# Performance work log

Measured on AMD Instinct MI355X. Metric: run time of the kernel, lower is better.

Reference implementation:

```python
import jax, jax.numpy as jnp
import numpy as np

HEAD_SIZE = 128
NUM_EMBED = 1024
BLOCK_SIZE = 2048


def setup_inputs() -> dict:
    key = jax.random.key(0)
    kx, kk, kq, kv = jax.random.split(key, 4)
    x = jax.random.normal(kx, (4, BLOCK_SIZE, NUM_EMBED), dtype=jnp.float32)
    s = 1.0 / np.sqrt(NUM_EMBED)
    Wk = jax.random.normal(kk, (NUM_EMBED, HEAD_SIZE), dtype=jnp.float32) * s
    Wq = jax.random.normal(kq, (NUM_EMBED, HEAD_SIZE), dtype=jnp.float32) * s
    Wv = jax.random.normal(kv, (NUM_EMBED, HEAD_SIZE), dtype=jnp.float32) * s
    return {"x": x, "Wk": Wk, "Wq": Wq, "Wv": Wv}


def reference(x, Wk, Wq, Wv):
    # x: [B, T, C]; W*: [C, H]
    B, T, C = x.shape
    k = x @ Wk          # [B, T, H]
    q = x @ Wq          # [B, T, H]
    v = x @ Wv          # [B, T, H]
    scale = k.shape[-1] ** -0.5
    wei = jnp.einsum('bth,bsh->bts', q, k) * scale  # [B, T, T]
    causal = jnp.tril(jnp.ones((T, T), dtype=bool))
    wei = jnp.where(causal, wei, -jnp.inf)
    wei = jax.nn.softmax(wei, axis=-1)
    out = jnp.einsum('bts,bsh->bth', wei, v)        # [B, T, H]
    return out
```

## Files before the change

### kernel.cpp

```cpp
#include <hip/hip_runtime.h>
#include <hip/hip_bf16.h>
#include <math.h>

#define B_ 4
#define T_ 2048
#define C_ 1024
#define H_ 128
#define SCALE 0.088388347648318447f

typedef unsigned short u16;
typedef __bf16 bf16x8 __attribute__((ext_vector_type(8)));
typedef __bf16 bf16x4 __attribute__((ext_vector_type(4)));
typedef float  f32x4  __attribute__((ext_vector_type(4)));
typedef u16    u16x8  __attribute__((ext_vector_type(8)));
typedef u16    u16x4  __attribute__((ext_vector_type(4)));

#define PO_OFF  0u
#define ML_OFF  18874368u
#define WBT_OFF 19169280u
#define QB_OFF  19955712u
#define KB_OFF  22052864u
#define VT_OFF  24150016u

__device__ __forceinline__ u16 f2bf(float f) {
    __hip_bfloat16 h = __float2bfloat16(f);
    return __builtin_bit_cast(u16, h);
}

__device__ __forceinline__ void load_lds16(const void* g, void* l) {
    __builtin_amdgcn_global_load_lds(
        (const __attribute__((address_space(1))) unsigned int*)g,
        (__attribute__((address_space(3))) unsigned int*)l, 16, 0, 0);
}

__global__ __launch_bounds__(256) void convert_w(const float* __restrict__ Wq,
                                                 const float* __restrict__ Wk,
                                                 const float* __restrict__ Wv,
                                                 u16* __restrict__ wbT) {
    const int id = blockIdx.x * 256 + threadIdx.x;
    const int s = id >> 17;
    const int r = id & 131071;
    const int k = r >> 7, n = r & 127;
    const float* W = (s == 0) ? Wq : (s == 1) ? Wk : Wv;
    float v = W[k * 128 + n];
    if (s == 0) v *= SCALE;
    wbT[(s << 17) + (n << 10) + k] = f2bf(v);
}

__global__ __launch_bounds__(256) void gemm_qkv(
    const float* __restrict__ x, const u16* __restrict__ wbT,
    u16* __restrict__ qb, u16* __restrict__ kb, u16* __restrict__ vT)
{
    __shared__ u16 xs[2][4096];
    __shared__ u16 ws[2][8192];

    const int tid = threadIdx.x;
    const int w = tid >> 6, lane = tid & 63, lg = lane >> 4, lr = lane & 15;
    const int wm = w >> 1, wn = w & 1;
    const int s = blockIdx.y;
    const int m0 = blockIdx.x * 64;
    const u16* wsrc = wbT + (s << 17);

    const int xrow = tid >> 2;
    const int xseg = tid & 3;
    const float* xbase = x + (size_t)(m0 + xrow) * C_ + xseg * 16;
    const unsigned xsw = ((unsigned)xrow & 7u) << 4;

    unsigned wro[4], wco[4];
#pragma unroll
    for (int i = 0; i < 4; ++i) {
        const unsigned o = (unsigned)(w * 4 + i) * 1024u + (unsigned)lane * 16u;
        const unsigned o2 = o ^ (((o >> 7) & 7u) << 4);
        wro[i] = o2 >> 7; wco[i] = (o2 & 127u) >> 1;
    }

    f32x4 acc[2][4] = {};

    {
        const float4 f0 = ((const float4*)xbase)[0], f1 = ((const float4*)xbase)[1];
        const float4 f2 = ((const float4*)xbase)[2], f3 = ((const float4*)xbase)[3];
#pragma unroll
        for (int i = 0; i < 4; ++i)
            load_lds16(wsrc + (size_t)wro[i] * C_ + wco[i], &ws[0][(w * 4 + i) * 512]);
        u16x8 lo, hi;
        lo[0] = f2bf(f0.x); lo[1] = f2bf(f0.y); lo[2] = f2bf(f0.z); lo[3] = f2bf(f0.w);
        lo[4] = f2bf(f1.x); lo[5] = f2bf(f1.y); lo[6] = f2bf(f1.z); lo[7] = f2bf(f1.w);
        hi[0] = f2bf(f2.x); hi[1] = f2bf(f2.y); hi[2] = f2bf(f2.z); hi[3] = f2bf(f2.w);
        hi[4] = f2bf(f3.x); hi[5] = f2bf(f3.y); hi[6] = f2bf(f3.z); hi[7] = f2bf(f3.w);
        char* rb = (char*)xs[0] + xrow * 128;
        *(u16x8*)(rb + (((unsigned)xseg * 32 + 0) ^ xsw)) = lo;
        *(u16x8*)(rb + (((unsigned)xseg * 32 + 16) ^ xsw)) = hi;
    }
    __syncthreads();

    int buf = 0;
    for (int k0 = 0; k0 < C_; k0 += 64) {
        const bool pf = (k0 + 64 < C_);
        float4 g0, g1, g2, g3;
        if (pf) {
            const float* xn = xbase + k0 + 64;
            g0 = ((const float4*)xn)[0]; g1 = ((const float4*)xn)[1];
            g2 = ((const float4*)xn)[2]; g3 = ((const float4*)xn)[3];
#pragma unroll
            for (int i = 0; i < 4; ++i)
                load_lds16(wsrc + (size_t)wro[i] * C_ + (k0 + 64) + wco[i],
                           &ws[buf ^ 1][(w * 4 + i) * 512]);
        }

#pragma unroll
        for (int kc = 0; kc < 2; ++kc) {
            bf16x8 af[2], bfr[4];
#pragma unroll
            for (int mi = 0; mi < 2; ++mi) {
                const int row = wm * 32 + mi * 16 + lr;
                const unsigned byte = (unsigned)(kc * 64 + lg * 16) ^ (((unsigned)row & 7u) << 4);
                af[mi] = *(const bf16x8*)((const char*)xs[buf] + row * 128 + byte);
            }
#pragma unroll
            for (int ni = 0; ni < 4; ++ni) {
                const int n = wn * 64 + ni * 16 + lr;
                const unsigned byte = (unsigned)(kc * 64 + lg * 16) ^ (((unsigned)n & 7u) << 4);
                bfr[ni] = *(const bf16x8*)((const char*)ws[buf] + n * 128 + byte);
            }
#pragma unroll
            for (int mi = 0; mi < 2; ++mi)
#pragma unroll
                for (int ni = 0; ni < 4; ++ni)
                    acc[mi][ni] = __builtin_amdgcn_mfma_f32_16x16x32_bf16(
                        af[mi], bfr[ni], acc[mi][ni], 0, 0, 0);
        }

        if (pf) {
            u16x8 lo, hi;
            lo[0] = f2bf(g0.x); lo[1] = f2bf(g0.y); lo[2] = f2bf(g0.z); lo[3] = f2bf(g0.w);
            lo[4] = f2bf(g1.x); lo[5] = f2bf(g1.y); lo[6] = f2bf(g1.z); lo[7] = f2bf(g1.w);
            hi[0] = f2bf(g2.x); hi[1] = f2bf(g2.y); hi[2] = f2bf(g2.z); hi[3] = f2bf(g2.w);
            hi[4] = f2bf(g3.x); hi[5] = f2bf(g3.y); hi[6] = f2bf(g3.z); hi[7] = f2bf(g3.w);
            char* rb = (char*)xs[buf ^ 1] + xrow * 128;
            *(u16x8*)(rb + (((unsigned)xseg * 32 + 0) ^ xsw)) = lo;
            *(u16x8*)(rb + (((unsigned)xseg * 32 + 16) ^ xsw)) = hi;
        }
        __syncthreads();
        buf ^= 1;
    }

    if (s < 2) {
        u16* dst = (s == 0) ? qb : kb;
#pragma unroll
        for (int mi = 0; mi < 2; ++mi)
#pragma unroll
            for (int ni = 0; ni < 4; ++ni) {
                const int trow = m0 + wm * 32 + mi * 16 + lg * 4;
                const int col = wn * 64 + ni * 16 + lr;
#pragma unroll
                for (int r = 0; r < 4; ++r)
                    dst[(size_t)(trow + r) * H_ + col] = f2bf(acc[mi][ni][r]);
            }
    } else {
#pragma unroll
        for (int mi = 0; mi < 2; ++mi)
#pragma unroll
            for (int ni = 0; ni < 4; ++ni) {
                const int trow = m0 + wm * 32 + mi * 16 + lg * 4;
                const int bb = trow >> 11, t = trow & 2047;
                const int d = wn * 64 + ni * 16 + lr;
                u16x4 pk;
                pk[0] = f2bf(acc[mi][ni][0]); pk[1] = f2bf(acc[mi][ni][1]);
                pk[2] = f2bf(acc[mi][ni][2]); pk[3] = f2bf(acc[mi][ni][3]);
                *(u16x4*)&vT[((size_t)bb * 128 + d) * 2048 + t] = pk;
            }
    }
}

__global__ __launch_bounds__(256) void attn_split(
    const u16* __restrict__ qb, const u16* __restrict__ kb,
    const u16* __restrict__ vT, float* __restrict__ po, float* __restrict__ ml)
{
    __shared__ u16 ks[2][4096];
    __shared__ u16 vs[2][128 * 36];

    const int jt = blockIdx.x, sp = blockIdx.y, b = blockIdx.z;
    const int kt0 = sp * 8;
    const int ktend_all = 2 * jt + 2;
    if (kt0 >= ktend_all) return;
    const int kt_end = min(kt0 + 8, ktend_all);

    const int tid = threadIdx.x;
    const int w = tid >> 6, lane = tid & 63, lg = lane >> 4, lr = lane & 15;
    const int qrow_base = jt * 64 + w * 16;

    const u16* kbB = kb + ((size_t)(b << 11)) * H_;
    const u16* vbB = vT + (size_t)b * 128 * 2048;

    unsigned krow[2], kcolb[2];
#pragma unroll
    for (int i = 0; i < 2; ++i) {
        const unsigned o_ = (unsigned)(w * 2 + i) * 1024u + (unsigned)lane * 16u;
        const unsigned o2 = o_ ^ (((o_ >> 8) & 7u) << 4);
        krow[i] = o2 >> 8; kcolb[i] = o2 & 255u;
    }
    int vd[2], vc[2];
#pragma unroll
    for (int i = 0; i < 2; ++i) {
        const int idx = i * 256 + tid;
        vd[i] = idx >> 2; vc[i] = idx & 3;
    }

    const u16* qp = qb + ((size_t)(b << 11) + qrow_base + lr) * H_;
    bf16x8 qf[4];
#pragma unroll
    for (int kc = 0; kc < 4; ++kc)
        qf[kc] = *(const bf16x8*)&qp[kc * 32 + lg * 8];

    u16x8 vr[2];
    {
        const u16* kbase = kbB + (size_t)kt0 * 32 * H_;
#pragma unroll
        for (int i = 0; i < 2; ++i)
            load_lds16((const char*)kbase + krow[i] * 256 + kcolb[i], &ks[0][(w * 2 + i) * 512]);
        const u16* vbase = vbB + (size_t)kt0 * 32;
#pragma unroll
        for (int i = 0; i < 2; ++i)
            vr[i] = *(const u16x8*)&vbase[(size_t)vd[i] * 2048 + vc[i] * 8];
#pragma unroll
        for (int i = 0; i < 2; ++i) {
            char* rb = (char*)vs[0] + vd[i] * 72 + (vc[i] & 2) * 4;
            *(u16x4*)(rb + ((2 * vc[i]) & 3) * 16)     = __builtin_shufflevector(vr[i], vr[i], 0, 1, 2, 3);
            *(u16x4*)(rb + ((2 * vc[i] + 1) & 3) * 16) = __builtin_shufflevector(vr[i], vr[i], 4, 5, 6, 7);
        }
    }
    __syncthreads();

    f32x4 o[8] = {};
    float m_run = -INFINITY, l_run = 0.f;
    int cur = 0;

    for (int kt = kt0; kt < kt_end; ++kt) {
        const bool pf = (kt + 1 < kt_end);
        if (pf) {
            const u16* kbase = kbB + (size_t)(kt + 1) * 32 * H_;
#pragma unroll
            for (int i = 0; i < 2; ++i)
                load_lds16((const char*)kbase + krow[i] * 256 + kcolb[i],
                           &ks[cur ^ 1][(w * 2 + i) * 512]);
            const u16* vbase = vbB + (size_t)(kt + 1) * 32;
#pragma unroll
            for (int i = 0; i < 2; ++i)
                vr[i] = *(const u16x8*)&vbase[(size_t)vd[i] * 2048 + vc[i] * 8];
        }

        f32x4 s0 = {0.f, 0.f, 0.f, 0.f}, s1 = {0.f, 0.f, 0.f, 0.f};
        const unsigned swz = ((unsigned)lr & 7u) << 4;
#pragma unroll
        for (int kc = 0; kc < 4; ++kc) {
            const unsigned byte = ((unsigned)(kc * 64 + lg * 16)) ^ swz;
            const bf16x8 kf0 = *(const bf16x8*)((const char*)ks[cur] + lr * 256 + byte);
            const bf16x8 kf1 = *(const bf16x8*)((const char*)ks[cur] + lr * 256 + 4096 + byte);
            s0 = __builtin_amdgcn_mfma_f32_16x16x32_bf16(kf0, qf[kc], s0, 0, 0, 0);
            s1 = __builtin_amdgcn_mfma_f32_16x16x32_bf16(kf1, qf[kc], s1, 0, 0, 0);
        }

        if (kt * 32 + 31 > qrow_base) {
            const int qg = qrow_base + lr;
            const int kvb = kt * 32 + lg * 4;
#pragma unroll
            for (int r = 0; r < 4; ++r) {
                if (kvb + r > qg)      s0[r] = -INFINITY;
                if (kvb + 16 + r > qg) s1[r] = -INFINITY;
            }
        }

        float mt = fmaxf(fmaxf(fmaxf(s0[0], s0[1]), fmaxf(s0[2], s0[3])),
                         fmaxf(fmaxf(s1[0], s1[1]), fmaxf(s1[2], s1[3])));
        mt = fmaxf(mt, __shfl_xor(mt, 16));
        mt = fmaxf(mt, __shfl_xor(mt, 32));
        const float mn = fmaxf(fmaxf(m_run, mt), -1e30f);
        const float p0 = __expf(s0[0] - mn), p1 = __expf(s0[1] - mn);
        const float p2 = __expf(s0[2] - mn), p3 = __expf(s0[3] - mn);
        const float p4 = __expf(s1[0] - mn), p5 = __expf(s1[1] - mn);
        const float p6 = __expf(s1[2] - mn), p7 = __expf(s1[3] - mn);
        float sum = ((p0 + p1) + (p2 + p3)) + ((p4 + p5) + (p6 + p7));
        sum += __shfl_xor(sum, 16);
        sum += __shfl_xor(sum, 32);
        const float f = __expf(m_run - mn);
        l_run = l_run * f + sum;
        m_run = mn;

        const float fb0 = __shfl(f, lg * 4 + 0);
        const float fb1 = __shfl(f, lg * 4 + 1);
        const float fb2 = __shfl(f, lg * 4 + 2);
        const float fb3 = __shfl(f, lg * 4 + 3);
#pragma unroll
        for (int ni = 0; ni < 8; ++ni) {
            o[ni][0] *= fb0; o[ni][1] *= fb1; o[ni][2] *= fb2; o[ni][3] *= fb3;
        }

        bf16x8 pa;
        pa[0] = (__bf16)p0; pa[1] = (__bf16)p1; pa[2] = (__bf16)p2; pa[3] = (__bf16)p3;
        pa[4] = (__bf16)p4; pa[5] = (__bf16)p5; pa[6] = (__bf16)p6; pa[7] = (__bf16)p7;

#pragma unroll
        for (int ni = 0; ni < 8; ++ni) {
            const bf16x8 vf = *(const bf16x8*)((const char*)vs[cur] + (ni * 16 + lr) * 72 + lg * 16);
            o[ni] = __builtin_amdgcn_mfma_f32_16x16x32_bf16(pa, vf, o[ni], 0, 0, 0);
        }

        if (pf) {
#pragma unroll
            for (int i = 0; i < 2; ++i) {
                char* rb = (char*)vs[cur ^ 1] + vd[i] * 72 + (vc[i] & 2) * 4;
                *(u16x4*)(rb + ((2 * vc[i]) & 3) * 16)     = __builtin_shufflevector(vr[i], vr[i], 0, 1, 2, 3);
                *(u16x4*)(rb + ((2 * vc[i] + 1) & 3) * 16) = __builtin_shufflevector(vr[i], vr[i], 4, 5, 6, 7);
            }
        }
        __syncthreads();
        cur ^= 1;
    }

    const int a = jt >> 2, b3 = jt & 3;
    const int slot = (a + 1) * (2 * a + b3) + sp;
    float* pob = po + (size_t)(b * 144 + slot) * 64 * 128;
#pragma unroll
    for (int ni = 0; ni < 8; ++ni) {
        const int col = ni * 16 + lr;
#pragma unroll
        for (int rj = 0; rj < 4; ++rj)
            pob[(w * 16 + lg * 4 + rj) * 128 + col] = o[ni][rj];
    }
    if (lg == 0) {
        float* mlb = ml + (size_t)(b * 144 + slot) * 128;
        mlb[w * 16 + lr] = m_run;
        mlb[64 + w * 16 + lr] = l_run;
    }
}

__global__ __launch_bounds__(256) void attn_combine(
    const float* __restrict__ po, const float* __restrict__ ml,
    float* __restrict__ out)
{
    const int rid = (blockIdx.x << 3) + (threadIdx.x >> 5);
    const int b = blockIdx.y;
    const int d4 = (threadIdx.x & 31) * 4;
    const int jt = rid >> 6, row = rid & 63;
    const int a = jt >> 2, b3 = jt & 3;
    const int slot0 = (a + 1) * (2 * a + b3);
    const int c = a + 1;

    float M = -INFINITY;
#pragma unroll
    for (int si = 0; si < 8; ++si)
        if (si < c) M = fmaxf(M, ml[(size_t)(b * 144 + slot0 + si) * 128 + row]);

    float L = 0.f;
    float a0 = 0.f, a1 = 0.f, a2 = 0.f, a3 = 0.f;
#pragma unroll
    for (int si = 0; si < 8; ++si) {
        if (si < c) {
            const float* mlb = ml + (size_t)(b * 144 + slot0 + si) * 128;
            const float wgt = __expf(mlb[row] - M);
            L += wgt * mlb[64 + row];
            const float4 t = *(const float4*)&po[((size_t)(b * 144 + slot0 + si) * 64 + row) * 128 + d4];
            a0 = fmaf(wgt, t.x, a0); a1 = fmaf(wgt, t.y, a1);
            a2 = fmaf(wgt, t.z, a2); a3 = fmaf(wgt, t.w, a3);
        }
    }
    const float inv = 1.f / L;
    *(float4*)&out[((size_t)(b << 11) + rid) * H_ + d4] =
        make_float4(a0 * inv, a1 * inv, a2 * inv, a3 * inv);
}

extern "C" void kernel_launch(void* const* d_in, const int* in_sizes, int n_in,
                              void* d_out, int out_size, void* d_ws, size_t ws_size,
                              hipStream_t stream) {
    const float* x  = (const float*)d_in[0];
    const float* Wk = (const float*)d_in[1];
    const float* Wq = (const float*)d_in[2];
    const float* Wv = (const float*)d_in[3];
    float* out = (float*)d_out;

    float* po = (float*)((char*)d_ws + PO_OFF);
    float* ml = (float*)((char*)d_ws + ML_OFF);
    u16* wbT  = (u16*)((char*)d_ws + WBT_OFF);
    u16* qb   = (u16*)((char*)d_ws + QB_OFF);
    u16* kb   = (u16*)((char*)d_ws + KB_OFF);
    u16* vT   = (u16*)((char*)d_ws + VT_OFF);

    convert_w<<<1536, 256, 0, stream>>>(Wq, Wk, Wv, wbT);
    gemm_qkv<<<dim3(128, 3), 256, 0, stream>>>(x, wbT, qb, kb, vT);
    attn_split<<<dim3(32, 8, 4), 256, 0, stream>>>(qb, kb, vT, po, ml);
    attn_combine<<<dim3(256, 4), 256, 0, stream>>>(po, ml, out);
}
```

Baseline: 67.66 us.

## Halve QKV GEMM row tile and add lazy softmax rescaling in attention

```diff
diff --git a/kernel.cpp b/kernel.cpp
--- a/kernel.cpp
+++ b/kernel.cpp
@@ -51,19 +51,19 @@
     const float* __restrict__ x, const u16* __restrict__ wbT,
     u16* __restrict__ qb, u16* __restrict__ kb, u16* __restrict__ vT)
 {
-    __shared__ u16 xs[2][4096];
+    __shared__ u16 xs[2][2048];
     __shared__ u16 ws[2][8192];
 
     const int tid = threadIdx.x;
     const int w = tid >> 6, lane = tid & 63, lg = lane >> 4, lr = lane & 15;
     const int wm = w >> 1, wn = w & 1;
     const int s = blockIdx.y;
-    const int m0 = blockIdx.x * 64;
+    const int m0 = blockIdx.x * 32;
     const u16* wsrc = wbT + (s << 17);
 
-    const int xrow = tid >> 2;
-    const int xseg = tid & 3;
-    const float* xbase = x + (size_t)(m0 + xrow) * C_ + xseg * 16;
+    const int xrow = tid >> 3;
+    const int xseg = tid & 7;
+    const float* xbase = x + (size_t)(m0 + xrow) * C_ + xseg * 8;
     const unsigned xsw = ((unsigned)xrow & 7u) << 4;
 
     unsigned wro[4], wco[4];
@@ -74,71 +74,55 @@
         wro[i] = o2 >> 7; wco[i] = (o2 & 127u) >> 1;
     }
 
-    f32x4 acc[2][4] = {};
+    f32x4 acc[4] = {};
 
     {
         const float4 f0 = ((const float4*)xbase)[0], f1 = ((const float4*)xbase)[1];
-        const float4 f2 = ((const float4*)xbase)[2], f3 = ((const float4*)xbase)[3];
 #pragma unroll
         for (int i = 0; i < 4; ++i)
             load_lds16(wsrc + (size_t)wro[i] * C_ + wco[i], &ws[0][(w * 4 + i) * 512]);
-        u16x8 lo, hi;
-        lo[0] = f2bf(f0.x); lo[1] = f2bf(f0.y); lo[2] = f2bf(f0.z); lo[3] = f2bf(f0.w);
-        lo[4] = f2bf(f1.x); lo[5] = f2bf(f1.y); lo[6] = f2bf(f1.z); lo[7] = f2bf(f1.w);
-        hi[0] = f2bf(f2.x); hi[1] = f2bf(f2.y); hi[2] = f2bf(f2.z); hi[3] = f2bf(f2.w);
-        hi[4] = f2bf(f3.x); hi[5] = f2bf(f3.y); hi[6] = f2bf(f3.z); hi[7] = f2bf(f3.w);
-        char* rb = (char*)xs[0] + xrow * 128;
-        *(u16x8*)(rb + (((unsigned)xseg * 32 + 0) ^ xsw)) = lo;
-        *(u16x8*)(rb + (((unsigned)xseg * 32 + 16) ^ xsw)) = hi;
+        u16x8 pk;
+        pk[0] = f2bf(f0.x); pk[1] = f2bf(f0.y); pk[2] = f2bf(f0.z); pk[3] = f2bf(f0.w);
+        pk[4] = f2bf(f1.x); pk[5] = f2bf(f1.y); pk[6] = f2bf(f1.z); pk[7] = f2bf(f1.w);
+        *(u16x8*)((char*)xs[0] + xrow * 128 + (((unsigned)xseg * 16) ^ xsw)) = pk;
     }
     __syncthreads();
 
     int buf = 0;
     for (int k0 = 0; k0 < C_; k0 += 64) {
         const bool pf = (k0 + 64 < C_);
-        float4 g0, g1, g2, g3;
+        float4 g0, g1;
         if (pf) {
             const float* xn = xbase + k0 + 64;
             g0 = ((const float4*)xn)[0]; g1 = ((const float4*)xn)[1];
-            g2 = ((const float4*)xn)[2]; g3 = ((const float4*)xn)[3];
 #pragma unroll
             for (int i = 0; i < 4; ++i)
                 load_lds16(wsrc + (size_t)wro[i] * C_ + (k0 + 64) + wco[i],
                            &ws[buf ^ 1][(w * 4 + i) * 512]);
         }
 
+        const int arow = wm * 16 + lr;
+        const unsigned asw = ((unsigned)arow & 7u) << 4;
 #pragma unroll
         for (int kc = 0; kc < 2; ++kc) {
-            bf16x8 af[2], bfr[4];
-#pragma unroll
-            for (int mi = 0; mi < 2; ++mi) {
-                const int row = wm * 32 + mi * 16 + lr;
-                const unsigned byte = (unsigned)(kc * 64 + lg * 16) ^ (((unsigned)row & 7u) << 4);
-                af[mi] = *(const bf16x8*)((const char*)xs[buf] + row * 128 + byte);
-            }
+            const unsigned kb_ = (unsigned)(kc * 64 + lg * 16);
+            const bf16x8 af = *(const bf16x8*)((const char*)xs[buf] + arow * 128 + (kb_ ^ asw));
+            bf16x8 bfr[4];
 #pragma unroll
             for (int ni = 0; ni < 4; ++ni) {
                 const int n = wn * 64 + ni * 16 + lr;
-                const unsigned byte = (unsigned)(kc * 64 + lg * 16) ^ (((unsigned)n & 7u) << 4);
-                bfr[ni] = *(const bf16x8*)((const char*)ws[buf] + n * 128 + byte);
+                bfr[ni] = *(const bf16x8*)((const char*)ws[buf] + n * 128 + (kb_ ^ (((unsigned)n & 7u) << 4)));
             }
 #pragma unroll
-            for (int mi = 0; mi < 2; ++mi)
-#pragma unroll
-                for (int ni = 0; ni < 4; ++ni)
-                    acc[mi][ni] = __builtin_amdgcn_mfma_f32_16x16x32_bf16(
-                        af[mi], bfr[ni], acc[mi][ni], 0, 0, 0);
+            for (int ni = 0; ni < 4; ++ni)
+                acc[ni] = __builtin_amdgcn_mfma_f32_16x16x32_bf16(af, bfr[ni], acc[ni], 0, 0, 0);
         }
 
         if (pf) {
-            u16x8 lo, hi;
-            lo[0] = f2bf(g0.x); lo[1] = f2bf(g0.y); lo[2] = f2bf(g0.z); lo[3] = f2bf(g0.w);
-            lo[4] = f2bf(g1.x); lo[5] = f2bf(g1.y); lo[6] = f2bf(g1.z); lo[7] = f2bf(g1.w);
-            hi[0] = f2bf(g2.x); hi[1] = f2bf(g2.y); hi[2] = f2bf(g2.z); hi[3] = f2bf(g2.w);
-            hi[4] = f2bf(g3.x); hi[5] = f2bf(g3.y); hi[6] = f2bf(g3.z); hi[7] = f2bf(g3.w);
-            char* rb = (char*)xs[buf ^ 1] + xrow * 128;
-            *(u16x8*)(rb + (((unsigned)xseg * 32 + 0) ^ xsw)) = lo;
-            *(u16x8*)(rb + (((unsigned)xseg * 32 + 16) ^ xsw)) = hi;
+            u16x8 pk;
+            pk[0] = f2bf(g0.x); pk[1] = f2bf(g0.y); pk[2] = f2bf(g0.z); pk[3] = f2bf(g0.w);
+            pk[4] = f2bf(g1.x); pk[5] = f2bf(g1.y); pk[6] = f2bf(g1.z); pk[7] = f2bf(g1.w);
+            *(u16x8*)((char*)xs[buf ^ 1] + xrow * 128 + (((unsigned)xseg * 16) ^ xsw)) = pk;
         }
         __syncthreads();
         buf ^= 1;
@@ -147,28 +131,24 @@
     if (s < 2) {
         u16* dst = (s == 0) ? qb : kb;
 #pragma unroll
-        for (int mi = 0; mi < 2; ++mi)
-#pragma unroll
-            for (int ni = 0; ni < 4; ++ni) {
-                const int trow = m0 + wm * 32 + mi * 16 + lg * 4;
-                const int col = wn * 64 + ni * 16 + lr;
-#pragma unroll
-                for (int r = 0; r < 4; ++r)
-                    dst[(size_t)(trow + r) * H_ + col] = f2bf(acc[mi][ni][r]);
-            }
+        for (int ni = 0; ni < 4; ++ni) {
+            const int trow = m0 + wm * 16 + lg * 4;
+            const int col = wn * 64 + ni * 16 + lr;
+#pragma unroll
+            for (int r = 0; r < 4; ++r)
+                dst[(size_t)(trow + r) * H_ + col] = f2bf(acc[ni][r]);
+        }
     } else {
 #pragma unroll
-        for (int mi = 0; mi < 2; ++mi)
-#pragma unroll
-            for (int ni = 0; ni < 4; ++ni) {
-                const int trow = m0 + wm * 32 + mi * 16 + lg * 4;
-                const int bb = trow >> 11, t = trow & 2047;
-                const int d = wn * 64 + ni * 16 + lr;
-                u16x4 pk;
-                pk[0] = f2bf(acc[mi][ni][0]); pk[1] = f2bf(acc[mi][ni][1]);
-                pk[2] = f2bf(acc[mi][ni][2]); pk[3] = f2bf(acc[mi][ni][3]);
-                *(u16x4*)&vT[((size_t)bb * 128 + d) * 2048 + t] = pk;
-            }
+        for (int ni = 0; ni < 4; ++ni) {
+            const int trow = m0 + wm * 16 + lg * 4;
+            const int bb = trow >> 11, t = trow & 2047;
+            const int d = wn * 64 + ni * 16 + lr;
+            u16x4 pk;
+            pk[0] = f2bf(acc[ni][0]); pk[1] = f2bf(acc[ni][1]);
+            pk[2] = f2bf(acc[ni][2]); pk[3] = f2bf(acc[ni][3]);
+            *(u16x4*)&vT[((size_t)bb * 128 + d) * 2048 + t] = pk;
+        }
     }
 }
 
@@ -232,7 +212,7 @@
     __syncthreads();
 
     f32x4 o[8] = {};
-    float m_run = -INFINITY, l_run = 0.f;
+    float m_run = -1e30f, l_run = 0.f;
     int cur = 0;
 
     for (int kt = kt0; kt < kt_end; ++kt) {
@@ -274,26 +254,28 @@
                          fmaxf(fmaxf(s1[0], s1[1]), fmaxf(s1[2], s1[3])));
         mt = fmaxf(mt, __shfl_xor(mt, 16));
         mt = fmaxf(mt, __shfl_xor(mt, 32));
-        const float mn = fmaxf(fmaxf(m_run, mt), -1e30f);
-        const float p0 = __expf(s0[0] - mn), p1 = __expf(s0[1] - mn);
-        const float p2 = __expf(s0[2] - mn), p3 = __expf(s0[3] - mn);
-        const float p4 = __expf(s1[0] - mn), p5 = __expf(s1[1] - mn);
-        const float p6 = __expf(s1[2] - mn), p7 = __expf(s1[3] - mn);
+        if (__any(mt > m_run + 8.f)) {
+            const float mn = fmaxf(m_run, mt);
+            const float f = __expf(m_run - mn);
+            const float fb0 = __shfl(f, lg * 4 + 0);
+            const float fb1 = __shfl(f, lg * 4 + 1);
+            const float fb2 = __shfl(f, lg * 4 + 2);
+            const float fb3 = __shfl(f, lg * 4 + 3);
+#pragma unroll
+            for (int ni = 0; ni < 8; ++ni) {
+                o[ni][0] *= fb0; o[ni][1] *= fb1; o[ni][2] *= fb2; o[ni][3] *= fb3;
+            }
+            l_run *= f;
+            m_run = mn;
+        }
+        const float p0 = __expf(s0[0] - m_run), p1 = __expf(s0[1] - m_run);
+        const float p2 = __expf(s0[2] - m_run), p3 = __expf(s0[3] - m_run);
+        const float p4 = __expf(s1[0] - m_run), p5 = __expf(s1[1] - m_run);
+        const float p6 = __expf(s1[2] - m_run), p7 = __expf(s1[3] - m_run);
         float sum = ((p0 + p1) + (p2 + p3)) + ((p4 + p5) + (p6 + p7));
         sum += __shfl_xor(sum, 16);
         sum += __shfl_xor(sum, 32);
-        const float f = __expf(m_run - mn);
-        l_run = l_run * f + sum;
-        m_run = mn;
-
-        const float fb0 = __shfl(f, lg * 4 + 0);
-        const float fb1 = __shfl(f, lg * 4 + 1);
-        const float fb2 = __shfl(f, lg * 4 + 2);
-        const float fb3 = __shfl(f, lg * 4 + 3);
-#pragma unroll
-        for (int ni = 0; ni < 8; ++ni) {
-            o[ni][0] *= fb0; o[ni][1] *= fb1; o[ni][2] *= fb2; o[ni][3] *= fb3;
-        }
+        l_run += sum;
 
         bf16x8 pa;
         pa[0] = (__bf16)p0; pa[1] = (__bf16)p1; pa[2] = (__bf16)p2; pa[3] = (__bf16)p3;
@@ -386,7 +368,7 @@
     u16* vT   = (u16*)((char*)d_ws + VT_OFF);
 
     convert_w<<<1536, 256, 0, stream>>>(Wq, Wk, Wv, wbT);
-    gemm_qkv<<<dim3(128, 3), 256, 0, stream>>>(x, wbT, qb, kb, vT);
+    gemm_qkv<<<dim3(256, 3), 256, 0, stream>>>(x, wbT, qb, kb, vT);
     attn_split<<<dim3(32, 8, 4), 256, 0, stream>>>(qb, kb, vT, po, ml);
     attn_combine<<<dim3(256, 4), 256, 0, stream>>>(po, ml, out);
 }
```

After: 64.16 us. 5.2% less time.

## Triple-buffer async LDS loads with partial vmcnt waits and lazy softmax rescale

Applied to the files above, without the earlier changes.

```diff
diff --git a/kernel.cpp b/kernel.cpp
--- a/kernel.cpp
+++ b/kernel.cpp
@@ -32,6 +32,13 @@
         (const __attribute__((address_space(1))) unsigned int*)g,
         (__attribute__((address_space(3))) unsigned int*)l, 16, 0, 0);
 }
+
+#define BARRIER_ALLOW(N)                                                   \
+    do {                                                                   \
+        asm volatile("s_waitcnt vmcnt(" #N ") lgkmcnt(0)" ::: "memory");   \
+        __builtin_amdgcn_sched_barrier(0);                                 \
+        __builtin_amdgcn_s_barrier();                                      \
+    } while (0)
 
 __global__ __launch_bounds__(256) void convert_w(const float* __restrict__ Wq,
                                                  const float* __restrict__ Wk,
@@ -52,7 +59,7 @@
     u16* __restrict__ qb, u16* __restrict__ kb, u16* __restrict__ vT)
 {
     __shared__ u16 xs[2][4096];
-    __shared__ u16 ws[2][8192];
+    __shared__ u16 ws[3][8192];
 
     const int tid = threadIdx.x;
     const int w = tid >> 6, lane = tid & 63, lg = lane >> 4, lr = lane & 15;
@@ -79,9 +86,13 @@
     {
         const float4 f0 = ((const float4*)xbase)[0], f1 = ((const float4*)xbase)[1];
         const float4 f2 = ((const float4*)xbase)[2], f3 = ((const float4*)xbase)[3];
+        __builtin_amdgcn_sched_barrier(0);
 #pragma unroll
         for (int i = 0; i < 4; ++i)
             load_lds16(wsrc + (size_t)wro[i] * C_ + wco[i], &ws[0][(w * 4 + i) * 512]);
+#pragma unroll
+        for (int i = 0; i < 4; ++i)
+            load_lds16(wsrc + (size_t)wro[i] * C_ + 64 + wco[i], &ws[1][(w * 4 + i) * 512]);
         u16x8 lo, hi;
         lo[0] = f2bf(f0.x); lo[1] = f2bf(f0.y); lo[2] = f2bf(f0.z); lo[3] = f2bf(f0.w);
         lo[4] = f2bf(f1.x); lo[5] = f2bf(f1.y); lo[6] = f2bf(f1.z); lo[7] = f2bf(f1.w);
@@ -91,22 +102,30 @@
         *(u16x8*)(rb + (((unsigned)xseg * 32 + 0) ^ xsw)) = lo;
         *(u16x8*)(rb + (((unsigned)xseg * 32 + 16) ^ xsw)) = hi;
     }
-    __syncthreads();
-
-    int buf = 0;
-    for (int k0 = 0; k0 < C_; k0 += 64) {
-        const bool pf = (k0 + 64 < C_);
+    BARRIER_ALLOW(4);
+
+#pragma unroll
+    for (int j = 0; j < 16; ++j) {
+        const int k0 = j * 64;
+        const bool pfx = (j + 1 < 16);
+        const bool pfw = (j + 2 < 16);
         float4 g0, g1, g2, g3;
-        if (pf) {
+        if (pfx) {
             const float* xn = xbase + k0 + 64;
             g0 = ((const float4*)xn)[0]; g1 = ((const float4*)xn)[1];
             g2 = ((const float4*)xn)[2]; g3 = ((const float4*)xn)[3];
+        }
+        __builtin_amdgcn_sched_barrier(0);
+        if (pfw) {
+            const int wslot = (j + 2) % 3;
 #pragma unroll
             for (int i = 0; i < 4; ++i)
-                load_lds16(wsrc + (size_t)wro[i] * C_ + (k0 + 64) + wco[i],
-                           &ws[buf ^ 1][(w * 4 + i) * 512]);
-        }
-
+                load_lds16(wsrc + (size_t)wro[i] * C_ + (k0 + 128) + wco[i],
+                           &ws[wslot][(w * 4 + i) * 512]);
+        }
+
+        const u16* xsb = xs[j & 1];
+        const u16* wsb = ws[j % 3];
 #pragma unroll
         for (int kc = 0; kc < 2; ++kc) {
             bf16x8 af[2], bfr[4];
@@ -114,13 +133,13 @@
             for (int mi = 0; mi < 2; ++mi) {
                 const int row = wm * 32 + mi * 16 + lr;
                 const unsigned byte = (unsigned)(kc * 64 + lg * 16) ^ (((unsigned)row & 7u) << 4);
-                af[mi] = *(const bf16x8*)((const char*)xs[buf] + row * 128 + byte);
+                af[mi] = *(const bf16x8*)((const char*)xsb + row * 128 + byte);
             }
 #pragma unroll
             for (int ni = 0; ni < 4; ++ni) {
                 const int n = wn * 64 + ni * 16 + lr;
                 const unsigned byte = (unsigned)(kc * 64 + lg * 16) ^ (((unsigned)n & 7u) << 4);
-                bfr[ni] = *(const bf16x8*)((const char*)ws[buf] + n * 128 + byte);
+                bfr[ni] = *(const bf16x8*)((const char*)wsb + n * 128 + byte);
             }
 #pragma unroll
             for (int mi = 0; mi < 2; ++mi)
@@ -130,18 +149,18 @@
                         af[mi], bfr[ni], acc[mi][ni], 0, 0, 0);
         }
 
-        if (pf) {
+        if (pfx) {
             u16x8 lo, hi;
             lo[0] = f2bf(g0.x); lo[1] = f2bf(g0.y); lo[2] = f2bf(g0.z); lo[3] = f2bf(g0.w);
             lo[4] = f2bf(g1.x); lo[5] = f2bf(g1.y); lo[6] = f2bf(g1.z); lo[7] = f2bf(g1.w);
             hi[0] = f2bf(g2.x); hi[1] = f2bf(g2.y); hi[2] = f2bf(g2.z); hi[3] = f2bf(g2.w);
             hi[4] = f2bf(g3.x); hi[5] = f2bf(g3.y); hi[6] = f2bf(g3.z); hi[7] = f2bf(g3.w);
-            char* rb = (char*)xs[buf ^ 1] + xrow * 128;
+            char* rb = (char*)xs[(j + 1) & 1] + xrow * 128;
             *(u16x8*)(rb + (((unsigned)xseg * 32 + 0) ^ xsw)) = lo;
             *(u16x8*)(rb + (((unsigned)xseg * 32 + 16) ^ xsw)) = hi;
         }
-        __syncthreads();
-        buf ^= 1;
+        if (pfw) { BARRIER_ALLOW(4); }
+        else     { BARRIER_ALLOW(0); }
     }
 
     if (s < 2) {
@@ -176,7 +195,7 @@
     const u16* __restrict__ qb, const u16* __restrict__ kb,
     const u16* __restrict__ vT, float* __restrict__ po, float* __restrict__ ml)
 {
-    __shared__ u16 ks[2][4096];
+    __shared__ u16 ks[3][4096];
     __shared__ u16 vs[2][128 * 36];
 
     const int jt = blockIdx.x, sp = blockIdx.y, b = blockIdx.z;
@@ -184,6 +203,7 @@
     const int ktend_all = 2 * jt + 2;
     if (kt0 >= ktend_all) return;
     const int kt_end = min(kt0 + 8, ktend_all);
+    const int nt = kt_end - kt0;
 
     const int tid = threadIdx.x;
     const int w = tid >> 6, lane = tid & 63, lg = lane >> 4, lr = lane & 15;
@@ -214,14 +234,21 @@
 
     u16x8 vr[2];
     {
-        const u16* kbase = kbB + (size_t)kt0 * 32 * H_;
-#pragma unroll
-        for (int i = 0; i < 2; ++i)
-            load_lds16((const char*)kbase + krow[i] * 256 + kcolb[i], &ks[0][(w * 2 + i) * 512]);
         const u16* vbase = vbB + (size_t)kt0 * 32;
 #pragma unroll
         for (int i = 0; i < 2; ++i)
             vr[i] = *(const u16x8*)&vbase[(size_t)vd[i] * 2048 + vc[i] * 8];
+        __builtin_amdgcn_sched_barrier(0);
+        const u16* kb0 = kbB + (size_t)kt0 * 32 * H_;
+#pragma unroll
+        for (int i = 0; i < 2; ++i)
+            load_lds16((const char*)kb0 + krow[i] * 256 + kcolb[i], &ks[0][(w * 2 + i) * 512]);
+        if (nt > 1) {
+            const u16* kb1 = kbB + (size_t)(kt0 + 1) * 32 * H_;
+#pragma unroll
+            for (int i = 0; i < 2; ++i)
+                load_lds16((const char*)kb1 + krow[i] * 256 + kcolb[i], &ks[1][(w * 2 + i) * 512]);
+        }
 #pragma unroll
         for (int i = 0; i < 2; ++i) {
             char* rb = (char*)vs[0] + vd[i] * 72 + (vc[i] & 2) * 4;
@@ -229,33 +256,41 @@
             *(u16x4*)(rb + ((2 * vc[i] + 1) & 3) * 16) = __builtin_shufflevector(vr[i], vr[i], 4, 5, 6, 7);
         }
     }
-    __syncthreads();
+    if (nt > 1) { BARRIER_ALLOW(2); }
+    else        { BARRIER_ALLOW(0); }
 
     f32x4 o[8] = {};
-    float m_run = -INFINITY, l_run = 0.f;
-    int cur = 0;
-
-    for (int kt = kt0; kt < kt_end; ++kt) {
-        const bool pf = (kt + 1 < kt_end);
-        if (pf) {
-            const u16* kbase = kbB + (size_t)(kt + 1) * 32 * H_;
-#pragma unroll
-            for (int i = 0; i < 2; ++i)
-                load_lds16((const char*)kbase + krow[i] * 256 + kcolb[i],
-                           &ks[cur ^ 1][(w * 2 + i) * 512]);
+    float m_run = -1e30f, l_run = 0.f;
+    int rs = 0;
+
+    for (int j = 0; j < nt; ++j) {
+        const int kt = kt0 + j;
+        const bool pfv = (j + 1 < nt);
+        const bool pfk = (j + 2 < nt);
+        if (pfv) {
             const u16* vbase = vbB + (size_t)(kt + 1) * 32;
 #pragma unroll
             for (int i = 0; i < 2; ++i)
                 vr[i] = *(const u16x8*)&vbase[(size_t)vd[i] * 2048 + vc[i] * 8];
         }
+        __builtin_amdgcn_sched_barrier(0);
+        if (pfk) {
+            int wslot = rs + 2; if (wslot >= 3) wslot -= 3;
+            const u16* kbn = kbB + (size_t)(kt + 2) * 32 * H_;
+#pragma unroll
+            for (int i = 0; i < 2; ++i)
+                load_lds16((const char*)kbn + krow[i] * 256 + kcolb[i],
+                           &ks[wslot][(w * 2 + i) * 512]);
+        }
 
         f32x4 s0 = {0.f, 0.f, 0.f, 0.f}, s1 = {0.f, 0.f, 0.f, 0.f};
         const unsigned swz = ((unsigned)lr & 7u) << 4;
+        const u16* ksb = ks[rs];
 #pragma unroll
         for (int kc = 0; kc < 4; ++kc) {
             const unsigned byte = ((unsigned)(kc * 64 + lg * 16)) ^ swz;
-            const bf16x8 kf0 = *(const bf16x8*)((const char*)ks[cur] + lr * 256 + byte);
-            const bf16x8 kf1 = *(const bf16x8*)((const char*)ks[cur] + lr * 256 + 4096 + byte);
+            const bf16x8 kf0 = *(const bf16x8*)((const char*)ksb + lr * 256 + byte);
+            const bf16x8 kf1 = *(const bf16x8*)((const char*)ksb + lr * 256 + 4096 + byte);
             s0 = __builtin_amdgcn_mfma_f32_16x16x32_bf16(kf0, qf[kc], s0, 0, 0, 0);
             s1 = __builtin_amdgcn_mfma_f32_16x16x32_bf16(kf1, qf[kc], s1, 0, 0, 0);
         }
@@ -274,26 +309,28 @@
                          fmaxf(fmaxf(s1[0], s1[1]), fmaxf(s1[2], s1[3])));
         mt = fmaxf(mt, __shfl_xor(mt, 16));
         mt = fmaxf(mt, __shfl_xor(mt, 32));
-        const float mn = fmaxf(fmaxf(m_run, mt), -1e30f);
-        const float p0 = __expf(s0[0] - mn), p1 = __expf(s0[1] - mn);
-        const float p2 = __expf(s0[2] - mn), p3 = __expf(s0[3] - mn);
-        const float p4 = __expf(s1[0] - mn), p5 = __expf(s1[1] - mn);
-        const float p6 = __expf(s1[2] - mn), p7 = __expf(s1[3] - mn);
+        if (__any(mt > m_run + 8.f)) {
+            const float mn = fmaxf(m_run, mt);
+            const float f = __expf(m_run - mn);
+            const float fb0 = __shfl(f, lg * 4 + 0);
+            const float fb1 = __shfl(f, lg * 4 + 1);
+            const float fb2 = __shfl(f, lg * 4 + 2);
+            const float fb3 = __shfl(f, lg * 4 + 3);
+#pragma unroll
+            for (int ni = 0; ni < 8; ++ni) {
+                o[ni][0] *= fb0; o[ni][1] *= fb1; o[ni][2] *= fb2; o[ni][3] *= fb3;
+            }
+            l_run *= f;
+            m_run = mn;
+        }
+        const float p0 = __expf(s0[0] - m_run), p1 = __expf(s0[1] - m_run);
+        const float p2 = __expf(s0[2] - m_run), p3 = __expf(s0[3] - m_run);
+        const float p4 = __expf(s1[0] - m_run), p5 = __expf(s1[1] - m_run);
+        const float p6 = __expf(s1[2] - m_run), p7 = __expf(s1[3] - m_run);
         float sum = ((p0 + p1) + (p2 + p3)) + ((p4 + p5) + (p6 + p7));
         sum += __shfl_xor(sum, 16);
         sum += __shfl_xor(sum, 32);
-        const float f = __expf(m_run - mn);
-        l_run = l_run * f + sum;
-        m_run = mn;
-
-        const float fb0 = __shfl(f, lg * 4 + 0);
-        const float fb1 = __shfl(f, lg * 4 + 1);
-        const float fb2 = __shfl(f, lg * 4 + 2);
-        const float fb3 = __shfl(f, lg * 4 + 3);
-#pragma unroll
-        for (int ni = 0; ni < 8; ++ni) {
-            o[ni][0] *= fb0; o[ni][1] *= fb1; o[ni][2] *= fb2; o[ni][3] *= fb3;
-        }
+        l_run += sum;
 
         bf16x8 pa;
         pa[0] = (__bf16)p0; pa[1] = (__bf16)p1; pa[2] = (__bf16)p2; pa[3] = (__bf16)p3;
@@ -301,20 +338,22 @@
 
 #pragma unroll
         for (int ni = 0; ni < 8; ++ni) {
-            const bf16x8 vf = *(const bf16x8*)((const char*)vs[cur] + (ni * 16 + lr) * 72 + lg * 16);
+            const bf16x8 vf = *(const bf16x8*)((const char*)vs[j & 1] + (ni * 16 + lr) * 72 + lg * 16);
             o[ni] = __builtin_amdgcn_mfma_f32_16x16x32_bf16(pa, vf, o[ni], 0, 0, 0);
         }
 
-        if (pf) {
+        if (pfv) {
 #pragma unroll
             for (int i = 0; i < 2; ++i) {
-                char* rb = (char*)vs[cur ^ 1] + vd[i] * 72 + (vc[i] & 2) * 4;
+                char* rb = (char*)vs[(j + 1) & 1] + vd[i] * 72 + (vc[i] & 2) * 4;
                 *(u16x4*)(rb + ((2 * vc[i]) & 3) * 16)     = __builtin_shufflevector(vr[i], vr[i], 0, 1, 2, 3);
                 *(u16x4*)(rb + ((2 * vc[i] + 1) & 3) * 16) = __builtin_shufflevector(vr[i], vr[i], 4, 5, 6, 7);
             }
         }
-        __syncthreads();
-        cur ^= 1;
+        if (pfk) { BARRIER_ALLOW(2); }
+        else     { BARRIER_ALLOW(0); }
+
+        rs = rs + 1; if (rs >= 3) rs -= 3;
     }
 
     const int a = jt >> 2, b3 = jt & 3;
```

After: 66.20 us. 1.02x faster.
